# Kernel optimization log

Measured on AMD Instinct MI355X. Metric: run time of the kernel, lower is better.

## Reference

```python
import jax, jax.numpy as jnp
import numpy as np

N_FEAT = 11   # players+ball features
HID = 48      # GAT hidden dim
HEADS = 4
GRU = 64
B = 64        # chains
T = 16        # frames per chain
NPG = 23      # nodes per frame graph (22 players + ball)
G = B * T
NTOT = G * NPG
FRAME = 2 * HID  # mean||max pool


def setup_inputs() -> dict:
    key = jax.random.key(0)
    ks = jax.random.split(key, 24)
    # block-diagonal fully-connected (with self loops) edge_index per graph
    base = np.arange(NPG)
    src = np.repeat(base, NPG)
    dst = np.tile(base, NPG)
    off = (np.arange(G) * NPG)[:, None]
    edge_index = np.stack([(src[None] + off).ravel(), (dst[None] + off).ravel()]).astype(np.int64)
    batch = np.repeat(np.arange(G), NPG).astype(np.int64)

    def p(k, shape, scale=0.1):
        return jax.random.normal(k, shape, jnp.float32) * scale

    return dict(
        x=jax.random.normal(ks[0], (NTOT, N_FEAT), jnp.float32),
        edge_index=jnp.asarray(edge_index), batch=jnp.asarray(batch),
        W1=p(ks[1], (N_FEAT, HEADS * HID)), as1=p(ks[2], (HEADS, HID)), ad1=p(ks[3], (HEADS, HID)), b1=p(ks[4], (HEADS * HID,)),
        W2=p(ks[5], (HEADS * HID, HID)), as2=p(ks[6], (1, HID)), ad2=p(ks[7], (1, HID)), b2=p(ks[8], (HID,)),
        Wih0=p(ks[9], (3 * GRU, FRAME)), Whh0=p(ks[10], (3 * GRU, GRU)), bih0=p(ks[11], (3 * GRU,)), bhh0=p(ks[12], (3 * GRU,)),
        Wih1=p(ks[13], (3 * GRU, GRU)), Whh1=p(ks[14], (3 * GRU, GRU)), bih1=p(ks[15], (3 * GRU,)), bhh1=p(ks[16], (3 * GRU,)),
        Wh1=p(ks[17], (GRU, 32)), bh1=p(ks[18], (32,)), Wh2=p(ks[19], (32, 1)), bh2=p(ks[20], (1,)),
    )


def _gat(x, src, dst, W, a_s, a_d, b, heads, concat):
    # PyG GATConv: per-head linear, edge score LeakyReLU(a_s.h_i + a_d.h_j),
    # softmax over incoming edges (by dst), weighted aggregation of h_src.
    h = (x @ W).reshape(-1, heads, HID)            # [N,H,D]
    al_s = (h * a_s).sum(-1)                       # [N,H]
    al_d = (h * a_d).sum(-1)
    e = jax.nn.leaky_relu(al_s[src] + al_d[dst], 0.2)  # [E,H]
    m = jax.ops.segment_max(e, dst, num_segments=NTOT)
    w = jnp.exp(e - m[dst])
    s = jax.ops.segment_sum(w, dst, num_segments=NTOT)
    alpha = w / (s[dst] + 1e-16)
    out = jax.ops.segment_sum(h[src] * alpha[:, :, None], dst, num_segments=NTOT)  # [N,H,D]
    if concat:
        return out.reshape(NTOT, heads * HID) + b
    return out.mean(1) + b


def _gru_layer(xs, Wih, Whh, bih, bhh):
    # torch.nn.GRU single layer, batch_first; xs: [B,T,in]
    def step(h, x_t):
        gi = x_t @ Wih.T + bih
        gh = h @ Whh.T + bhh
        ir, iz, in_ = jnp.split(gi, 3, -1)
        hr, hz, hn = jnp.split(gh, 3, -1)
        r = jax.nn.sigmoid(ir + hr)
        z = jax.nn.sigmoid(iz + hz)
        n = jnp.tanh(in_ + r * hn)
        h2 = (1 - z) * n + z * h
        return h2, h2
    h0 = jnp.zeros((xs.shape[0], GRU), xs.dtype)
    _, out = jax.lax.scan(step, h0, jnp.swapaxes(xs, 0, 1))
    return jnp.swapaxes(out, 0, 1)


def reference(x, edge_index, batch, W1, as1, ad1, b1, W2, as2, ad2, b2,
              Wih0, Whh0, bih0, bhh0, Wih1, Whh1, bih1, bhh1, Wh1, bh1, Wh2, bh2):
    src, dst = edge_index[0], edge_index[1]
    h = jax.nn.elu(_gat(x, src, dst, W1, as1, ad1, b1, HEADS, True))   # [N,192]
    h = jax.nn.elu(_gat(h, src, dst, W2, as2, ad2, b2, 1, False))      # [N,48]
    mean = jax.ops.segment_sum(h, batch, num_segments=G) / NPG
    mx = jax.ops.segment_max(h, batch, num_segments=G)
    frames = jnp.concatenate([mean, mx], -1).reshape(B, T, FRAME)      # [B,T,96]
    h1 = _gru_layer(frames, Wih0, Whh0, bih0, bhh0)
    h2 = _gru_layer(h1, Wih1, Whh1, bih1, bhh1)
    last = h2[:, -1]                                                   # [B,64]
    logits = jax.nn.relu(last @ Wh1 + bh1) @ Wh2 + bh2                 # [B,1]
    return logits[:, 0]
```

## Files before the change

### kernel.cpp

```cpp
#include <hip/hip_runtime.h>
#include <math.h>

#define NPG    23
#define HID    48
#define HEADS  4
#define C1     192
#define NFEAT  11
#define GG     1024
#define GRUH   64
#define FRAME  96
#define TT     16
#define BB     64

#define HSTR   196
#define GSTR   52

#define OFF_X    0
#define OFF_ALS  256
#define OFF_ALD  348
#define OFF_H    440
#define OFF_H1   4948
#define LDSF     9456

__device__ __forceinline__ float elu_(float v) {
    return (v > 0.f) ? v : (__expf(v) - 1.f);
}

__global__ __launch_bounds__(256, 4) void gat_fused(
    const float* __restrict__ x,
    const float* __restrict__ W1,
    const float* __restrict__ as1,
    const float* __restrict__ ad1,
    const float* __restrict__ b1,
    const float* __restrict__ W2,
    const float* __restrict__ as2,
    const float* __restrict__ ad2,
    const float* __restrict__ b2,
    const float* __restrict__ Wih0,
    const float* __restrict__ bih0,
    float* __restrict__ gi0)
{
    __shared__ float S[LDSF];
    float* s_x    = S + OFF_X;
    float* s_als  = S + OFF_ALS;
    float* s_ald  = S + OFF_ALD;
    float* s_h    = S + OFF_H;
    float* s_h1   = S + OFF_H1;
    float* s_gA   = S + OFF_H;
    float* s_gB   = S + OFF_H + NPG * GSTR;
    float* s_h2   = S + OFF_H + 2 * NPG * GSTR;
    float* s_als2 = S + OFF_X;
    float* s_ald2 = S + OFF_X + NPG;
    float* s_frame= S + OFF_X;

    const int g   = blockIdx.x;
    const int tid = threadIdx.x;

    for (int i = tid; i < NPG * NFEAT; i += 256) s_x[i] = x[g * NPG * NFEAT + i];
    __syncthreads();

    if (tid < 240) {
        const int c4 = tid % 48, ng = tid / 48;
        float4 acc[5];
        #pragma unroll
        for (int nn = 0; nn < 5; nn++) acc[nn] = make_float4(0.f, 0.f, 0.f, 0.f);
        #pragma unroll
        for (int k = 0; k < NFEAT; k++) {
            const float4 w = *(const float4*)(W1 + k * C1 + 4 * c4);
            #pragma unroll
            for (int nn = 0; nn < 5; nn++) {
                int n = ng * 5 + nn; n = (n < NPG) ? n : NPG - 1;
                const float xv = s_x[n * NFEAT + k];
                acc[nn].x += xv * w.x; acc[nn].y += xv * w.y;
                acc[nn].z += xv * w.z; acc[nn].w += xv * w.w;
            }
        }
        #pragma unroll
        for (int nn = 0; nn < 5; nn++) {
            const int n = ng * 5 + nn;
            if (n < NPG) *(float4*)(s_h + n * HSTR + 4 * c4) = acc[nn];
        }
    }
    __syncthreads();

    if (tid < 184) {
        const int which = tid / 92, r = tid % 92, hh = r / NPG, n = r % NPG;
        const float* av = (which ? ad1 : as1) + hh * HID;
        const float* hp = s_h + n * HSTR + hh * HID;
        float s = 0.f;
        #pragma unroll
        for (int k4 = 0; k4 < 12; k4++) {
            const float4 h4 = *(const float4*)(hp + 4 * k4);
            const float4 a4 = *(const float4*)(av + 4 * k4);
            s += h4.x * a4.x + h4.y * a4.y + h4.z * a4.z + h4.w * a4.w;
        }
        if (which) s_ald[hh * NPG + n] = s; else s_als[hh * NPG + n] = s;
    }
    __syncthreads();

    if (tid < 184) {
        const int j = tid >> 3, sub = tid & 7;
        const int hh = sub >> 1, half = sub & 1;
        const float ald_j = s_ald[hh * NPG + j];
        float a[NPG];
        float m = -1e30f;
        #pragma unroll
        for (int i = 0; i < NPG; i++) {
            float e = s_als[hh * NPG + i] + ald_j;
            e = (e > 0.f) ? e : 0.2f * e;
            a[i] = e;
            m = fmaxf(m, e);
        }
        float ssum = 0.f;
        #pragma unroll
        for (int i = 0; i < NPG; i++) {
            const float w = __expf(a[i] - m);
            a[i] = w;
            ssum += w;
        }
        const float inv = 1.f / (ssum + 1e-16f);
        const int cb = hh * HID + half * 24;
        #pragma unroll
        for (int c4 = 0; c4 < 6; c4++) {
            float4 acc = make_float4(0.f, 0.f, 0.f, 0.f);
            #pragma unroll
            for (int i = 0; i < NPG; i++) {
                const float4 hv = *(const float4*)(s_h + i * HSTR + cb + 4 * c4);
                acc.x += a[i] * hv.x; acc.y += a[i] * hv.y;
                acc.z += a[i] * hv.z; acc.w += a[i] * hv.w;
            }
            const float4 bb = *(const float4*)(b1 + cb + 4 * c4);
            float4 v;
            v.x = elu_(acc.x * inv + bb.x);
            v.y = elu_(acc.y * inv + bb.y);
            v.z = elu_(acc.z * inv + bb.z);
            v.w = elu_(acc.w * inv + bb.w);
            *(float4*)(s_h1 + j * HSTR + cb + 4 * c4) = v;
        }
    }
    __syncthreads();

    if (tid < 144) {
        const int c4 = tid % 12, ng = (tid / 12) % 6, kc = tid / 72;
        float4 acc[4];
        #pragma unroll
        for (int nn = 0; nn < 4; nn++) acc[nn] = make_float4(0.f, 0.f, 0.f, 0.f);
        const int kbase = kc * 24;
        #pragma unroll 4
        for (int k4 = 0; k4 < 24; k4++) {
            const int kk = kbase + k4;
            const float* w2p = W2 + (4 * kk) * HID + 4 * c4;
            const float4 r0 = *(const float4*)(w2p);
            const float4 r1 = *(const float4*)(w2p + HID);
            const float4 r2 = *(const float4*)(w2p + 2 * HID);
            const float4 r3 = *(const float4*)(w2p + 3 * HID);
            #pragma unroll
            for (int nn = 0; nn < 4; nn++) {
                int n = ng * 4 + nn; n = (n < NPG) ? n : NPG - 1;
                const float4 hv = *(const float4*)(s_h1 + n * HSTR + 4 * kk);
                acc[nn].x += hv.x*r0.x + hv.y*r1.x + hv.z*r2.x + hv.w*r3.x;
                acc[nn].y += hv.x*r0.y + hv.y*r1.y + hv.z*r2.y + hv.w*r3.y;
                acc[nn].z += hv.x*r0.z + hv.y*r1.z + hv.z*r2.z + hv.w*r3.z;
                acc[nn].w += hv.x*r0.w + hv.y*r1.w + hv.z*r2.w + hv.w*r3.w;
            }
        }
        float* dstb = kc ? s_gB : s_gA;
        #pragma unroll
        for (int nn = 0; nn < 4; nn++) {
            const int n = ng * 4 + nn;
            if (n < NPG) *(float4*)(dstb + n * GSTR + 4 * c4) = acc[nn];
        }
    }
    __syncthreads();

    for (int task = tid; task < NPG * 12; task += 256) {
        const int n = task / 12, c4 = task % 12;
        const float4 a = *(const float4*)(s_gA + n * GSTR + 4 * c4);
        const float4 b = *(const float4*)(s_gB + n * GSTR + 4 * c4);
        *(float4*)(s_gA + n * GSTR + 4 * c4) =
            make_float4(a.x + b.x, a.y + b.y, a.z + b.z, a.w + b.w);
    }
    __syncthreads();

    if (tid < 46) {
        const int which = tid / NPG, n = tid % NPG;
        const float* av = which ? ad2 : as2;
        const float* gp = s_gA + n * GSTR;
        float s = 0.f;
        #pragma unroll
        for (int k4 = 0; k4 < 12; k4++) {
            const float4 g4 = *(const float4*)(gp + 4 * k4);
            const float4 a4 = *(const float4*)(av + 4 * k4);
            s += g4.x * a4.x + g4.y * a4.y + g4.z * a4.z + g4.w * a4.w;
        }
        if (which) s_ald2[n] = s; else s_als2[n] = s;
    }
    __syncthreads();

    if (tid < 92) {
        const int j = tid >> 2, q = tid & 3;
        const float ald_j = s_ald2[j];
        float a[NPG];
        float m = -1e30f;
        #pragma unroll
        for (int i = 0; i < NPG; i++) {
            float e = s_als2[i] + ald_j;
            e = (e > 0.f) ? e : 0.2f * e;
            a[i] = e;
            m = fmaxf(m, e);
        }
        float ssum = 0.f;
        #pragma unroll
        for (int i = 0; i < NPG; i++) {
            const float w = __expf(a[i] - m);
            a[i] = w;
            ssum += w;
        }
        const float inv = 1.f / (ssum + 1e-16f);
        #pragma unroll
        for (int c4 = 0; c4 < 3; c4++) {
            const int cb = q * 12 + 4 * c4;
            float4 acc = make_float4(0.f, 0.f, 0.f, 0.f);
            #pragma unroll
            for (int i = 0; i < NPG; i++) {
                const float4 gv = *(const float4*)(s_gA + i * GSTR + cb);
                acc.x += a[i] * gv.x; acc.y += a[i] * gv.y;
                acc.z += a[i] * gv.z; acc.w += a[i] * gv.w;
            }
            const float4 bb = *(const float4*)(b2 + cb);
            float4 v;
            v.x = elu_(acc.x * inv + bb.x);
            v.y = elu_(acc.y * inv + bb.y);
            v.z = elu_(acc.z * inv + bb.z);
            v.w = elu_(acc.w * inv + bb.w);
            *(float4*)(s_h2 + j * HID + cb) = v;
        }
    }
    __syncthreads();

    if (tid < HID) {
        float sm = 0.f, mx = -1e30f;
        #pragma unroll
        for (int j = 0; j < NPG; j++) {
            const float v = s_h2[j * HID + tid];
            sm += v; mx = fmaxf(mx, v);
        }
        s_frame[tid]       = sm * (1.0f / NPG);
        s_frame[HID + tid] = mx;
    }
    __syncthreads();

    if (tid < C1) {
        float s = bih0[tid];
        const float4* wr = (const float4*)(Wih0 + tid * FRAME);
        const float4* fr = (const float4*)s_frame;
        #pragma unroll
        for (int k4 = 0; k4 < FRAME / 4; k4++) {
            const float4 w = wr[k4];
            const float4 f = fr[k4];
            s += w.x * f.x + w.y * f.y + w.z * f.z + w.w * f.w;
        }
        gi0[g * C1 + tid] = s;
    }
}

__global__ __launch_bounds__(192) void gru_head(
    const float* __restrict__ gi0g,
    const float* __restrict__ Whh0,
    const float* __restrict__ bhh0,
    const float* __restrict__ Wih1,
    const float* __restrict__ bih1,
    const float* __restrict__ Whh1,
    const float* __restrict__ bhh1,
    const float* __restrict__ Wh1,
    const float* __restrict__ bh1,
    const float* __restrict__ Wh2,
    const float* __restrict__ bh2,
    float* __restrict__ out)
{
    __shared__ float s_gi0[TT * C1];
    __shared__ float s_h0[GRUH], s_h1[GRUH];
    __shared__ float s_gh0[C1], s_gi1[C1], s_gh1[C1];
    __shared__ float s_t1[32];

    const int b = blockIdx.x, tid = threadIdx.x;

    {
        const float4* src = (const float4*)(gi0g + b * TT * C1);
        float4* dst = (float4*)s_gi0;
        #pragma unroll
        for (int i = 0; i < 4; i++) dst[tid + 192 * i] = src[tid + 192 * i];
    }
    if (tid < GRUH) { s_h0[tid] = 0.f; s_h1[tid] = 0.f; }

    float w0[64], w1[64], w2[64];
    {
        const float4* p0 = (const float4*)(Whh0 + tid * 64);
        const float4* p1 = (const float4*)(Wih1 + tid * 64);
        const float4* p2 = (const float4*)(Whh1 + tid * 64);
        #pragma unroll
        for (int k4 = 0; k4 < 16; k4++) {
            const float4 v0 = p0[k4];
            w0[4*k4] = v0.x; w0[4*k4+1] = v0.y; w0[4*k4+2] = v0.z; w0[4*k4+3] = v0.w;
            const float4 v1 = p1[k4];
            w1[4*k4] = v1.x; w1[4*k4+1] = v1.y; w1[4*k4+2] = v1.z; w1[4*k4+3] = v1.w;
            const float4 v2 = p2[k4];
            w2[4*k4] = v2.x; w2[4*k4+1] = v2.y; w2[4*k4+2] = v2.z; w2[4*k4+3] = v2.w;
        }
    }
    const float bh0r = bhh0[tid], bi1r = bih1[tid], bh1r = bhh1[tid];
    __syncthreads();

    for (int it = 0; it <= TT; it++) {
        {
            float s0 = bh0r, s1 = bi1r, s2 = bh1r;
            const float4* h0v = (const float4*)s_h0;
            const float4* h1v = (const float4*)s_h1;
            #pragma unroll
            for (int k4 = 0; k4 < 16; k4++) {
                const float4 a = h0v[k4];
                const float4 c = h1v[k4];
                s0 += w0[4*k4]*a.x + w0[4*k4+1]*a.y + w0[4*k4+2]*a.z + w0[4*k4+3]*a.w;
                s1 += w1[4*k4]*a.x + w1[4*k4+1]*a.y + w1[4*k4+2]*a.z + w1[4*k4+3]*a.w;
                s2 += w2[4*k4]*c.x + w2[4*k4+1]*c.y + w2[4*k4+2]*c.z + w2[4*k4+3]*c.w;
            }
            s_gh0[tid] = s0; s_gi1[tid] = s1; s_gh1[tid] = s2;
        }
        __syncthreads();
        if (tid < GRUH) {
            if (it < TT) {
                const float ir = s_gi0[it*C1 + tid];
                const float iz = s_gi0[it*C1 + 64 + tid];
                const float in_ = s_gi0[it*C1 + 128 + tid];
                const float hr = s_gh0[tid], hz = s_gh0[64 + tid], hn = s_gh0[128 + tid];
                const float r = 1.f / (1.f + __expf(-(ir + hr)));
                const float z = 1.f / (1.f + __expf(-(iz + hz)));
                const float nx = in_ + r * hn;
                const float e2 = __expf(2.f * nx);
                const float n = (e2 - 1.f) / (e2 + 1.f);
                s_h0[tid] = (1.f - z) * n + z * s_h0[tid];
            }
        } else if (tid < 2 * GRUH) {
            if (it >= 1) {
                const int c = tid - GRUH;
                const float ir = s_gi1[c], iz = s_gi1[64 + c], in_ = s_gi1[128 + c];
                const float hr = s_gh1[c], hz = s_gh1[64 + c], hn = s_gh1[128 + c];
                const float r = 1.f / (1.f + __expf(-(ir + hr)));
                const float z = 1.f / (1.f + __expf(-(iz + hz)));
                const float nx = in_ + r * hn;
                const float e2 = __expf(2.f * nx);
                const float n = (e2 - 1.f) / (e2 + 1.f);
                s_h1[c] = (1.f - z) * n + z * s_h1[c];
            }
        }
        __syncthreads();
    }

    if (tid < 32) {
        float s = bh1[tid];
        #pragma unroll
        for (int k = 0; k < GRUH; k++) s += s_h1[k] * Wh1[k * 32 + tid];
        s_t1[tid] = fmaxf(s, 0.f);
    }
    __syncthreads();
    if (tid == 0) {
        float s = bh2[0];
        #pragma unroll
        for (int k = 0; k < 32; k++) s += s_t1[k] * Wh2[k];
        out[b] = s;
    }
}

extern "C" void kernel_launch(void* const* d_in, const int* in_sizes, int n_in,
                              void* d_out, int out_size, void* d_ws, size_t ws_size,
                              hipStream_t stream) {
    const float* x    = (const float*)d_in[0];
    const float* W1   = (const float*)d_in[3];
    const float* as1  = (const float*)d_in[4];
    const float* ad1  = (const float*)d_in[5];
    const float* b1   = (const float*)d_in[6];
    const float* W2   = (const float*)d_in[7];
    const float* as2  = (const float*)d_in[8];
    const float* ad2  = (const float*)d_in[9];
    const float* b2   = (const float*)d_in[10];
    const float* Wih0 = (const float*)d_in[11];
    const float* Whh0 = (const float*)d_in[12];
    const float* bih0 = (const float*)d_in[13];
    const float* bhh0 = (const float*)d_in[14];
    const float* Wih1 = (const float*)d_in[15];
    const float* Whh1 = (const float*)d_in[16];
    const float* bih1 = (const float*)d_in[17];
    const float* bhh1 = (const float*)d_in[18];
    const float* Wh1  = (const float*)d_in[19];
    const float* bh1  = (const float*)d_in[20];
    const float* Wh2  = (const float*)d_in[21];
    const float* bh2  = (const float*)d_in[22];

    float* out  = (float*)d_out;
    float* gi0  = (float*)d_ws;

    hipLaunchKernelGGL(gat_fused, dim3(GG), dim3(256), 0, stream,
                       x, W1, as1, ad1, b1, W2, as2, ad2, b2, Wih0, bih0, gi0);
    hipLaunchKernelGGL(gru_head, dim3(BB), dim3(192), 0, stream,
                       gi0, Whh0, bhh0, Wih1, bih1, Whh1, bhh1,
                       Wh1, bh1, Wh2, bh2, out);
}
```

Before: 61.49 us.

## Fuse GAT attention dots via LDS atomics and move Wih0 projection into GRU kernel

Attention score dot products for both GAT layers are now folded into the projection stages with shared-memory atomic adds, which removes separate passes and barriers. The second projection splits K four ways and reduces with lane shuffles instead of a separate LDS add pass. The layer-2 aggregation handles two nodes per thread. The Wih0 input projection moves from the per-graph kernel into the GRU kernel, which now uses 384 threads and splits each recurrent dot product across two lanes to shorten the serial step. The cost is LDS atomics, extra shuffles, and more work inside the 64-block GRU kernel.

```diff
diff --git a/kernel.cpp b/kernel.cpp
--- a/kernel.cpp
+++ b/kernel.cpp
@@ -36,9 +36,7 @@
     const float* __restrict__ as2,
     const float* __restrict__ ad2,
     const float* __restrict__ b2,
-    const float* __restrict__ Wih0,
-    const float* __restrict__ bih0,
-    float* __restrict__ gi0)
+    float* __restrict__ frames)
 {
     __shared__ float S[LDSF];
     float* s_x    = S + OFF_X;
@@ -46,55 +44,42 @@
     float* s_ald  = S + OFF_ALD;
     float* s_h    = S + OFF_H;
     float* s_h1   = S + OFF_H1;
-    float* s_gA   = S + OFF_H;
-    float* s_gB   = S + OFF_H + NPG * GSTR;
-    float* s_h2   = S + OFF_H + 2 * NPG * GSTR;
+    float* s_g    = S + OFF_H;
+    float* s_h2   = S + OFF_H + NPG * GSTR;
     float* s_als2 = S + OFF_X;
     float* s_ald2 = S + OFF_X + NPG;
-    float* s_frame= S + OFF_X;
 
     const int g   = blockIdx.x;
     const int tid = threadIdx.x;
 
     for (int i = tid; i < NPG * NFEAT; i += 256) s_x[i] = x[g * NPG * NFEAT + i];
+    if (tid < 184) s_als[tid] = 0.f;
     __syncthreads();
 
     if (tid < 240) {
         const int c4 = tid % 48, ng = tid / 48;
-        float4 acc[5];
-        #pragma unroll
-        for (int nn = 0; nn < 5; nn++) acc[nn] = make_float4(0.f, 0.f, 0.f, 0.f);
-        #pragma unroll
-        for (int k = 0; k < NFEAT; k++) {
-            const float4 w = *(const float4*)(W1 + k * C1 + 4 * c4);
-            #pragma unroll
-            for (int nn = 0; nn < 5; nn++) {
-                int n = ng * 5 + nn; n = (n < NPG) ? n : NPG - 1;
-                const float xv = s_x[n * NFEAT + k];
-                acc[nn].x += xv * w.x; acc[nn].y += xv * w.y;
-                acc[nn].z += xv * w.z; acc[nn].w += xv * w.w;
-            }
-        }
+        const int hh = c4 / 12;
+        const float4 a_s = *(const float4*)(as1 + 4 * c4);
+        const float4 a_d = *(const float4*)(ad1 + 4 * c4);
         #pragma unroll
         for (int nn = 0; nn < 5; nn++) {
             const int n = ng * 5 + nn;
-            if (n < NPG) *(float4*)(s_h + n * HSTR + 4 * c4) = acc[nn];
-        }
-    }
-    __syncthreads();
-
-    if (tid < 184) {
-        const int which = tid / 92, r = tid % 92, hh = r / NPG, n = r % NPG;
-        const float* av = (which ? ad1 : as1) + hh * HID;
-        const float* hp = s_h + n * HSTR + hh * HID;
-        float s = 0.f;
-        #pragma unroll
-        for (int k4 = 0; k4 < 12; k4++) {
-            const float4 h4 = *(const float4*)(hp + 4 * k4);
-            const float4 a4 = *(const float4*)(av + 4 * k4);
-            s += h4.x * a4.x + h4.y * a4.y + h4.z * a4.z + h4.w * a4.w;
-        }
-        if (which) s_ald[hh * NPG + n] = s; else s_als[hh * NPG + n] = s;
+            if (n < NPG) {
+                float4 acc = make_float4(0.f, 0.f, 0.f, 0.f);
+                #pragma unroll
+                for (int k = 0; k < NFEAT; k++) {
+                    const float4 w = *(const float4*)(W1 + k * C1 + 4 * c4);
+                    const float xv = s_x[n * NFEAT + k];
+                    acc.x += xv * w.x; acc.y += xv * w.y;
+                    acc.z += xv * w.z; acc.w += xv * w.w;
+                }
+                *(float4*)(s_h + n * HSTR + 4 * c4) = acc;
+                atomicAdd(&s_als[hh * NPG + n],
+                          acc.x * a_s.x + acc.y * a_s.y + acc.z * a_s.z + acc.w * a_s.w);
+                atomicAdd(&s_ald[hh * NPG + n],
+                          acc.x * a_d.x + acc.y * a_d.y + acc.z * a_d.z + acc.w * a_d.w);
+            }
+        }
     }
     __syncthreads();
 
@@ -137,26 +122,29 @@
             v.w = elu_(acc.w * inv + bb.w);
             *(float4*)(s_h1 + j * HSTR + cb + 4 * c4) = v;
         }
-    }
-    __syncthreads();
-
-    if (tid < 144) {
-        const int c4 = tid % 12, ng = (tid / 12) % 6, kc = tid / 72;
-        float4 acc[4];
-        #pragma unroll
-        for (int nn = 0; nn < 4; nn++) acc[nn] = make_float4(0.f, 0.f, 0.f, 0.f);
-        const int kbase = kc * 24;
-        #pragma unroll 4
-        for (int k4 = 0; k4 < 24; k4++) {
-            const int kk = kbase + k4;
+    } else if (tid < 184 + 46) {
+        s_als2[tid - 184] = 0.f;
+    }
+    __syncthreads();
+
+    if (tid < 192) {
+        const int kc  = tid & 3;
+        const int rem = tid >> 2;
+        const int c4  = rem % 12, ng = rem / 12;
+        float4 acc[6];
+        #pragma unroll
+        for (int nn = 0; nn < 6; nn++) acc[nn] = make_float4(0.f, 0.f, 0.f, 0.f);
+        #pragma unroll 2
+        for (int k4 = 0; k4 < 12; k4++) {
+            const int kk = kc * 12 + k4;
             const float* w2p = W2 + (4 * kk) * HID + 4 * c4;
             const float4 r0 = *(const float4*)(w2p);
             const float4 r1 = *(const float4*)(w2p + HID);
             const float4 r2 = *(const float4*)(w2p + 2 * HID);
             const float4 r3 = *(const float4*)(w2p + 3 * HID);
             #pragma unroll
-            for (int nn = 0; nn < 4; nn++) {
-                int n = ng * 4 + nn; n = (n < NPG) ? n : NPG - 1;
+            for (int nn = 0; nn < 6; nn++) {
+                int n = ng * 6 + nn; n = (n < NPG) ? n : NPG - 1;
                 const float4 hv = *(const float4*)(s_h1 + n * HSTR + 4 * kk);
                 acc[nn].x += hv.x*r0.x + hv.y*r1.x + hv.z*r2.x + hv.w*r3.x;
                 acc[nn].y += hv.x*r0.y + hv.y*r1.y + hv.z*r2.y + hv.w*r3.y;
@@ -164,76 +152,90 @@
                 acc[nn].w += hv.x*r0.w + hv.y*r1.w + hv.z*r2.w + hv.w*r3.w;
             }
         }
-        float* dstb = kc ? s_gB : s_gA;
-        #pragma unroll
-        for (int nn = 0; nn < 4; nn++) {
-            const int n = ng * 4 + nn;
-            if (n < NPG) *(float4*)(dstb + n * GSTR + 4 * c4) = acc[nn];
-        }
-    }
-    __syncthreads();
-
-    for (int task = tid; task < NPG * 12; task += 256) {
-        const int n = task / 12, c4 = task % 12;
-        const float4 a = *(const float4*)(s_gA + n * GSTR + 4 * c4);
-        const float4 b = *(const float4*)(s_gB + n * GSTR + 4 * c4);
-        *(float4*)(s_gA + n * GSTR + 4 * c4) =
-            make_float4(a.x + b.x, a.y + b.y, a.z + b.z, a.w + b.w);
-    }
-    __syncthreads();
-
-    if (tid < 46) {
-        const int which = tid / NPG, n = tid % NPG;
-        const float* av = which ? ad2 : as2;
-        const float* gp = s_gA + n * GSTR;
-        float s = 0.f;
-        #pragma unroll
-        for (int k4 = 0; k4 < 12; k4++) {
-            const float4 g4 = *(const float4*)(gp + 4 * k4);
-            const float4 a4 = *(const float4*)(av + 4 * k4);
-            s += g4.x * a4.x + g4.y * a4.y + g4.z * a4.z + g4.w * a4.w;
-        }
-        if (which) s_ald2[n] = s; else s_als2[n] = s;
-    }
-    __syncthreads();
-
-    if (tid < 92) {
-        const int j = tid >> 2, q = tid & 3;
-        const float ald_j = s_ald2[j];
-        float a[NPG];
-        float m = -1e30f;
+        #pragma unroll
+        for (int nn = 0; nn < 6; nn++) {
+            float4 a = acc[nn];
+            a.x += __shfl_xor(a.x, 1); a.x += __shfl_xor(a.x, 2);
+            a.y += __shfl_xor(a.y, 1); a.y += __shfl_xor(a.y, 2);
+            a.z += __shfl_xor(a.z, 1); a.z += __shfl_xor(a.z, 2);
+            a.w += __shfl_xor(a.w, 1); a.w += __shfl_xor(a.w, 2);
+            acc[nn] = a;
+        }
+        if (kc == 0) {
+            const float4 a_s = *(const float4*)(as2 + 4 * c4);
+            const float4 a_d = *(const float4*)(ad2 + 4 * c4);
+            #pragma unroll
+            for (int nn = 0; nn < 6; nn++) {
+                const int n = ng * 6 + nn;
+                if (n < NPG) {
+                    *(float4*)(s_g + n * GSTR + 4 * c4) = acc[nn];
+                    atomicAdd(&s_als2[n],
+                              acc[nn].x*a_s.x + acc[nn].y*a_s.y + acc[nn].z*a_s.z + acc[nn].w*a_s.w);
+                    atomicAdd(&s_ald2[n],
+                              acc[nn].x*a_d.x + acc[nn].y*a_d.y + acc[nn].z*a_d.z + acc[nn].w*a_d.w);
+                }
+            }
+        }
+    }
+    __syncthreads();
+
+    if (tid < 48) {
+        const int q = tid & 3, jp = tid >> 2;
+        const int j0 = 2 * jp, j1 = 2 * jp + 1;
+        const bool has1 = (j1 < NPG);
+        const int cb = q * 12;
+        const float ald0 = s_ald2[j0];
+        const float ald1 = has1 ? s_ald2[j1] : 0.f;
+        float m0 = -1e30f, m1 = -1e30f;
         #pragma unroll
         for (int i = 0; i < NPG; i++) {
-            float e = s_als2[i] + ald_j;
-            e = (e > 0.f) ? e : 0.2f * e;
-            a[i] = e;
-            m = fmaxf(m, e);
-        }
-        float ssum = 0.f;
+            const float ai = s_als2[i];
+            float e0 = ai + ald0; e0 = (e0 > 0.f) ? e0 : 0.2f * e0;
+            float e1 = ai + ald1; e1 = (e1 > 0.f) ? e1 : 0.2f * e1;
+            m0 = fmaxf(m0, e0); m1 = fmaxf(m1, e1);
+        }
+        float4 acc0[3], acc1[3];
+        #pragma unroll
+        for (int c = 0; c < 3; c++) {
+            acc0[c] = make_float4(0.f, 0.f, 0.f, 0.f);
+            acc1[c] = make_float4(0.f, 0.f, 0.f, 0.f);
+        }
+        float ss0 = 0.f, ss1 = 0.f;
         #pragma unroll
         for (int i = 0; i < NPG; i++) {
-            const float w = __expf(a[i] - m);
-            a[i] = w;
-            ssum += w;
-        }
-        const float inv = 1.f / (ssum + 1e-16f);
-        #pragma unroll
-        for (int c4 = 0; c4 < 3; c4++) {
-            const int cb = q * 12 + 4 * c4;
-            float4 acc = make_float4(0.f, 0.f, 0.f, 0.f);
-            #pragma unroll
-            for (int i = 0; i < NPG; i++) {
-                const float4 gv = *(const float4*)(s_gA + i * GSTR + cb);
-                acc.x += a[i] * gv.x; acc.y += a[i] * gv.y;
-                acc.z += a[i] * gv.z; acc.w += a[i] * gv.w;
-            }
-            const float4 bb = *(const float4*)(b2 + cb);
+            const float ai = s_als2[i];
+            float e0 = ai + ald0; e0 = (e0 > 0.f) ? e0 : 0.2f * e0;
+            float e1 = ai + ald1; e1 = (e1 > 0.f) ? e1 : 0.2f * e1;
+            const float p0 = __expf(e0 - m0); ss0 += p0;
+            const float p1 = __expf(e1 - m1); ss1 += p1;
+            const float* gp = s_g + i * GSTR + cb;
+            #pragma unroll
+            for (int c = 0; c < 3; c++) {
+                const float4 gv = *(const float4*)(gp + 4 * c);
+                acc0[c].x += p0 * gv.x; acc0[c].y += p0 * gv.y;
+                acc0[c].z += p0 * gv.z; acc0[c].w += p0 * gv.w;
+                acc1[c].x += p1 * gv.x; acc1[c].y += p1 * gv.y;
+                acc1[c].z += p1 * gv.z; acc1[c].w += p1 * gv.w;
+            }
+        }
+        const float inv0 = 1.f / (ss0 + 1e-16f);
+        const float inv1 = 1.f / (ss1 + 1e-16f);
+        #pragma unroll
+        for (int c = 0; c < 3; c++) {
+            const float4 bb = *(const float4*)(b2 + cb + 4 * c);
             float4 v;
-            v.x = elu_(acc.x * inv + bb.x);
-            v.y = elu_(acc.y * inv + bb.y);
-            v.z = elu_(acc.z * inv + bb.z);
-            v.w = elu_(acc.w * inv + bb.w);
-            *(float4*)(s_h2 + j * HID + cb) = v;
+            v.x = elu_(acc0[c].x * inv0 + bb.x);
+            v.y = elu_(acc0[c].y * inv0 + bb.y);
+            v.z = elu_(acc0[c].z * inv0 + bb.z);
+            v.w = elu_(acc0[c].w * inv0 + bb.w);
+            *(float4*)(s_h2 + j0 * HID + cb + 4 * c) = v;
+            if (has1) {
+                v.x = elu_(acc1[c].x * inv1 + bb.x);
+                v.y = elu_(acc1[c].y * inv1 + bb.y);
+                v.z = elu_(acc1[c].z * inv1 + bb.z);
+                v.w = elu_(acc1[c].w * inv1 + bb.w);
+                *(float4*)(s_h2 + j1 * HID + cb + 4 * c) = v;
+            }
         }
     }
     __syncthreads();
@@ -245,27 +247,15 @@
             const float v = s_h2[j * HID + tid];
             sm += v; mx = fmaxf(mx, v);
         }
-        s_frame[tid]       = sm * (1.0f / NPG);
-        s_frame[HID + tid] = mx;
-    }
-    __syncthreads();
-
-    if (tid < C1) {
-        float s = bih0[tid];
-        const float4* wr = (const float4*)(Wih0 + tid * FRAME);
-        const float4* fr = (const float4*)s_frame;
-        #pragma unroll
-        for (int k4 = 0; k4 < FRAME / 4; k4++) {
-            const float4 w = wr[k4];
-            const float4 f = fr[k4];
-            s += w.x * f.x + w.y * f.y + w.z * f.z + w.w * f.w;
-        }
-        gi0[g * C1 + tid] = s;
+        frames[g * FRAME + tid]       = sm * (1.0f / NPG);
+        frames[g * FRAME + HID + tid] = mx;
     }
 }
 
-__global__ __launch_bounds__(192) void gru_head(
-    const float* __restrict__ gi0g,
+__global__ __launch_bounds__(384) void gru_head(
+    const float* __restrict__ frames,
+    const float* __restrict__ Wih0,
+    const float* __restrict__ bih0,
     const float* __restrict__ Whh0,
     const float* __restrict__ bhh0,
     const float* __restrict__ Wih1,
@@ -278,6 +268,7 @@
     const float* __restrict__ bh2,
     float* __restrict__ out)
 {
+    __shared__ float s_f[TT * FRAME];
     __shared__ float s_gi0[TT * C1];
     __shared__ float s_h0[GRUH], s_h1[GRUH];
     __shared__ float s_gh0[C1], s_gi1[C1], s_gh1[C1];
@@ -286,20 +277,41 @@
     const int b = blockIdx.x, tid = threadIdx.x;
 
     {
-        const float4* src = (const float4*)(gi0g + b * TT * C1);
-        float4* dst = (float4*)s_gi0;
-        #pragma unroll
-        for (int i = 0; i < 4; i++) dst[tid + 192 * i] = src[tid + 192 * i];
+        const float4* src = (const float4*)(frames + b * TT * FRAME);
+        ((float4*)s_f)[tid] = src[tid];
     }
     if (tid < GRUH) { s_h0[tid] = 0.f; s_h1[tid] = 0.f; }
-
-    float w0[64], w1[64], w2[64];
+    __syncthreads();
+
     {
-        const float4* p0 = (const float4*)(Whh0 + tid * 64);
-        const float4* p1 = (const float4*)(Wih1 + tid * 64);
-        const float4* p2 = (const float4*)(Whh1 + tid * 64);
-        #pragma unroll
-        for (int k4 = 0; k4 < 16; k4++) {
+        const int c = tid % C1, tp = tid / C1;
+        float accg[8];
+        const float b0 = bih0[c];
+        #pragma unroll
+        for (int tt = 0; tt < 8; tt++) accg[tt] = b0;
+        const float4* wr = (const float4*)(Wih0 + c * FRAME);
+        const float4* f4 = (const float4*)s_f;
+        #pragma unroll 4
+        for (int k4 = 0; k4 < FRAME / 4; k4++) {
+            const float4 w = wr[k4];
+            #pragma unroll
+            for (int tt = 0; tt < 8; tt++) {
+                const float4 f = f4[(tt * 2 + tp) * (FRAME / 4) + k4];
+                accg[tt] += w.x * f.x + w.y * f.y + w.z * f.z + w.w * f.w;
+            }
+        }
+        #pragma unroll
+        for (int tt = 0; tt < 8; tt++) s_gi0[(tt * 2 + tp) * C1 + c] = accg[tt];
+    }
+
+    const int row = tid >> 1, kh = tid & 1;
+    float w0[32], w1[32], w2[32];
+    {
+        const float4* p0 = (const float4*)(Whh0 + row * 64 + kh * 32);
+        const float4* p1 = (const float4*)(Wih1 + row * 64 + kh * 32);
+        const float4* p2 = (const float4*)(Whh1 + row * 64 + kh * 32);
+        #pragma unroll
+        for (int k4 = 0; k4 < 8; k4++) {
             const float4 v0 = p0[k4];
             w0[4*k4] = v0.x; w0[4*k4+1] = v0.y; w0[4*k4+2] = v0.z; w0[4*k4+3] = v0.w;
             const float4 v1 = p1[k4];
@@ -308,23 +320,28 @@
             w2[4*k4] = v2.x; w2[4*k4+1] = v2.y; w2[4*k4+2] = v2.z; w2[4*k4+3] = v2.w;
         }
     }
-    const float bh0r = bhh0[tid], bi1r = bih1[tid], bh1r = bhh1[tid];
+    const float bh0r = kh ? 0.f : bhh0[row];
+    const float bi1r = kh ? 0.f : bih1[row];
+    const float bh1r = kh ? 0.f : bhh1[row];
     __syncthreads();
 
     for (int it = 0; it <= TT; it++) {
         {
             float s0 = bh0r, s1 = bi1r, s2 = bh1r;
-            const float4* h0v = (const float4*)s_h0;
-            const float4* h1v = (const float4*)s_h1;
-            #pragma unroll
-            for (int k4 = 0; k4 < 16; k4++) {
+            const float4* h0v = (const float4*)(s_h0 + kh * 32);
+            const float4* h1v = (const float4*)(s_h1 + kh * 32);
+            #pragma unroll
+            for (int k4 = 0; k4 < 8; k4++) {
                 const float4 a = h0v[k4];
                 const float4 c = h1v[k4];
                 s0 += w0[4*k4]*a.x + w0[4*k4+1]*a.y + w0[4*k4+2]*a.z + w0[4*k4+3]*a.w;
                 s1 += w1[4*k4]*a.x + w1[4*k4+1]*a.y + w1[4*k4+2]*a.z + w1[4*k4+3]*a.w;
                 s2 += w2[4*k4]*c.x + w2[4*k4+1]*c.y + w2[4*k4+2]*c.z + w2[4*k4+3]*c.w;
             }
-            s_gh0[tid] = s0; s_gi1[tid] = s1; s_gh1[tid] = s2;
+            s0 += __shfl_xor(s0, 1, 64);
+            s1 += __shfl_xor(s1, 1, 64);
+            s2 += __shfl_xor(s2, 1, 64);
+            if (kh == 0) { s_gh0[row] = s0; s_gi1[row] = s1; s_gh1[row] = s2; }
         }
         __syncthreads();
         if (tid < GRUH) {
@@ -396,12 +413,12 @@
     const float* Wh2  = (const float*)d_in[21];
     const float* bh2  = (const float*)d_in[22];
 
-    float* out  = (float*)d_out;
-    float* gi0  = (float*)d_ws;
+    float* out    = (float*)d_out;
+    float* frames = (float*)d_ws;
 
     hipLaunchKernelGGL(gat_fused, dim3(GG), dim3(256), 0, stream,
-                       x, W1, as1, ad1, b1, W2, as2, ad2, b2, Wih0, bih0, gi0);
-    hipLaunchKernelGGL(gru_head, dim3(BB), dim3(192), 0, stream,
-                       gi0, Whh0, bhh0, Wih1, bih1, Whh1, bhh1,
+                       x, W1, as1, ad1, b1, W2, as2, ad2, b2, frames);
+    hipLaunchKernelGGL(gru_head, dim3(BB), dim3(384), 0, stream,
+                       frames, Wih0, bih0, Whh0, bhh0, Wih1, bih1, Whh1, bhh1,
                        Wh1, bh1, Wh2, bh2, out);
 }
```

After: 106.5 us. +73.3%, slower.
